# Kernel optimization log

Hardware: AMD Instinct MI355X
Metric: run time of the kernel (lower is better)

## Reference

```python
import jax, jax.numpy as jnp
import numpy as np

E = 1024
H = 16
F = 4096
EPS = 1e-5


def layer_norm(x, gamma, beta):
    mu = jnp.mean(x, axis=-1, keepdims=True)
    var = jnp.var(x, axis=-1, keepdims=True)
    return (x - mu) * jax.lax.rsqrt(var + EPS) * gamma + beta


def setup_inputs() -> dict:
    key = jax.random.key(0)
    ks = jax.random.split(key, 12)
    s = lambda d: 1.0 / np.sqrt(d)
    x = jax.random.normal(ks[0], (2, 2048, E), dtype=jnp.float32)
    Wq = jax.random.uniform(ks[1], (E, E), minval=-s(E), maxval=s(E))
    bq = jnp.zeros((E,), jnp.float32)
    Wk = jax.random.uniform(ks[2], (E, E), minval=-s(E), maxval=s(E))
    bk = jnp.zeros((E,), jnp.float32)
    Wv = jax.random.uniform(ks[3], (E, E), minval=-s(E), maxval=s(E))
    bv = jnp.zeros((E,), jnp.float32)
    Wo = jax.random.uniform(ks[4], (E, E), minval=-s(E), maxval=s(E))
    bo = jnp.zeros((E,), jnp.float32)
    g1 = jnp.ones((E,), jnp.float32)
    b1 = jnp.zeros((E,), jnp.float32)
    W1 = jax.random.uniform(ks[5], (E, F), minval=-s(E), maxval=s(E))
    bf1 = jnp.zeros((F,), jnp.float32)
    W2 = jax.random.uniform(ks[6], (F, E), minval=-s(F), maxval=s(F))
    bf2 = jnp.zeros((E,), jnp.float32)
    g2 = jnp.ones((E,), jnp.float32)
    b2 = jnp.zeros((E,), jnp.float32)
    return dict(x=x, Wq=Wq, bq=bq, Wk=Wk, bk=bk, Wv=Wv, bv=bv, Wo=Wo, bo=bo,
                g1=g1, b1=b1, W1=W1, bf1=bf1, W2=W2, bf2=bf2, g2=g2, b2=b2)


def reference(x, Wq, bq, Wk, bk, Wv, bv, Wo, bo, g1, b1, W1, bf1, W2, bf2, g2, b2):
    B, L, _ = x.shape
    Dh = E // H
    q = (x @ Wq + bq).reshape(B, L, H, Dh).transpose(0, 2, 1, 3)  # b h l d
    k = (x @ Wk + bk).reshape(B, L, H, Dh).transpose(0, 2, 1, 3)  # computed but unused (faithful to source)
    v = (x @ Wv + bv).reshape(B, L, H, Dh).transpose(0, 2, 1, 3)
    # NOTE: source computes scores as Q @ V^T (not K), scaled, then softmax
    scores = jnp.einsum('bhqd,bhkd->bhqk', q, v) / jnp.sqrt(jnp.float32(Dh))
    att = jax.nn.softmax(scores, axis=-1)
    ctx = jnp.einsum('bhqk,bhkd->bhqd', att, v)
    ctx = ctx.transpose(0, 2, 1, 3).reshape(B, L, E)
    att_out = ctx @ Wo + bo
    post_att = layer_norm(x + att_out, g1, b1)
    ff = jax.nn.relu(post_att @ W1 + bf1) @ W2 + bf2
    return layer_norm(post_att + ff, g2, b2)
```

## Files before the change

kernel.cpp:

```cpp
#include <hip/hip_runtime.h>
#include <stdint.h>

typedef unsigned short u16;
typedef __attribute__((ext_vector_type(8))) short short8;
typedef __attribute__((ext_vector_type(4))) float f32x4;
typedef __attribute__((ext_vector_type(4))) unsigned short u16x4;

#define TOKENS 4096
#define E_DIM 1024
#define F_DIM 4096
#define SEQ 2048
#define NH 16
#define DH 64

__device__ __forceinline__ u16 f2b(float f) {
  union { float f; unsigned u; } v; v.f = f;
  unsigned r = v.u + 0x7fffu + ((v.u >> 16) & 1u);
  return (u16)(r >> 16);
}

__device__ __forceinline__ void gl2lds16(const u16* g, u16* l) {
  __builtin_amdgcn_global_load_lds(
      (const __attribute__((address_space(1))) unsigned int*)(size_t)(g),
      (__attribute__((address_space(3))) unsigned int*)(unsigned int)(size_t)(l),
      16, 0, 0);
}


__global__ __launch_bounds__(256)
void transpose_w(const float* __restrict__ W, u16* __restrict__ Wt, int K, int N) {
  __shared__ float tile[32][33];
  const int kb = blockIdx.x * 32, nb = blockIdx.y * 32;
  const int tx = threadIdx.x & 31, ty = threadIdx.x >> 5;
#pragma unroll
  for (int i = 0; i < 32; i += 8)
    tile[ty + i][tx] = W[(size_t)(kb + ty + i) * N + nb + tx];
  __syncthreads();
#pragma unroll
  for (int i = 0; i < 32; i += 8)
    Wt[(size_t)(nb + ty + i) * K + kb + tx] = f2b(tile[tx][ty + i]);
}

__global__ __launch_bounds__(256)
void f32_to_bf16(const float* __restrict__ in, u16* __restrict__ out) {
  const int i = blockIdx.x * 256 + threadIdx.x;
  f32x4 f = ((const f32x4*)in)[i];
  u16x4 u;
#pragma unroll
  for (int j = 0; j < 4; j++) u[j] = f2b(f[j]);
  ((u16x4*)out)[i] = u;
}

__global__ __launch_bounds__(256)
void transpose_v(const u16* __restrict__ vsrc, u16* __restrict__ vt) {
  __shared__ u16 tile[64][66];
  const int kb = blockIdx.x * 64;
  const int bh = blockIdx.y;
  const int b = bh >> 4, h = bh & 15;
  {
    const int d = threadIdx.x & 63, r = threadIdx.x >> 6;
#pragma unroll
    for (int i = 0; i < 64; i += 4)
      tile[r + i][d] = vsrc[(size_t)(b * SEQ + kb + r + i) * E_DIM + h * DH + d];
  }
  __syncthreads();
  {
    const int pos = threadIdx.x & 63;
    const int srck = (pos & 3) * 16 + (pos >> 2);
#pragma unroll
    for (int j = 0; j < 64; j += 4) {
      const int d = (threadIdx.x >> 6) + j;
      vt[(size_t)(bh * DH + d) * SEQ + kb + pos] = tile[srck][d];
    }
  }
}

template <int RELU, int OUTBF>
__global__ __launch_bounds__(512)
void gemm256(const u16* __restrict__ A, const u16* __restrict__ Bt,
             const float* __restrict__ bias, void* __restrict__ Cout,
             int N, int K) {
  __shared__ __align__(16) u16 lds[3][2][8192];
  const int tid = threadIdx.x;
  const int lane = tid & 63, wave = tid >> 6;
  const int wm = wave >> 2, wn = wave & 3;
  const int l15 = lane & 15, g = lane >> 4;

  const int bid = blockIdx.x;
  const int xcd = bid & 7, idx = bid >> 3;
  const int mT = (xcd >> 2) * 8 + (idx >> 2);
  const int nT = (xcd & 3) * 4 + (idx & 3);
  const int mBlk = mT * 256, nBlk = nT * 256;

  const u16* Ab = A + (size_t)mBlk * K;
  const u16* Bb = Bt + (size_t)nBlk * K;

  const int srow = lane >> 2;
  const int scolx = ((lane & 3) ^ ((lane >> 3) & 3)) * 8;
  const u16* sa0 = Ab + (size_t)(wave * 16 + srow) * K + scolx;
  const u16* sa1 = Ab + (size_t)((8 + wave) * 16 + srow) * K + scolx;
  const u16* sb0 = Bb + (size_t)(wave * 16 + srow) * K + scolx;
  const u16* sb1 = Bb + (size_t)((8 + wave) * 16 + srow) * K + scolx;

  const int fo = l15 * 32 + ((g ^ ((l15 >> 1) & 3)) << 3);

  f32x4 acc[8][4] = {};

  const int NT = K >> 5;

#define STAGE_A(buf, t)                                             \
  {                                                                 \
    gl2lds16(sa0 + (size_t)(t) * 32, &lds[buf][0][wave * 512 + lane * 8]);       \
    gl2lds16(sa1 + (size_t)(t) * 32, &lds[buf][0][(8 + wave) * 512 + lane * 8]); \
  }
#define STAGE_B(buf, t)                                             \
  {                                                                 \
    gl2lds16(sb0 + (size_t)(t) * 32, &lds[buf][1][wave * 512 + lane * 8]);       \
    gl2lds16(sb1 + (size_t)(t) * 32, &lds[buf][1][(8 + wave) * 512 + lane * 8]); \
  }

  STAGE_A(0, 0) STAGE_B(0, 0)
  STAGE_A(1, 1) STAGE_B(1, 1)
  asm volatile("s_waitcnt vmcnt(4)" ::: "memory");
  asm volatile("s_barrier" ::: "memory");

  int buf = 0, sbuf = 2;
  for (int t = 0; t < NT; ++t) {
    const u16* As_ = &lds[buf][0][wm * (8 * 512)];
    const u16* Bs_ = &lds[buf][1][wn * (4 * 512)];

    short8 af[4], bfr[4];
#pragma unroll
    for (int i = 0; i < 4; i++)
      af[i] = *(const short8*)(As_ + i * 512 + fo);
#pragma unroll
    for (int i = 0; i < 4; i++)
      bfr[i] = *(const short8*)(Bs_ + i * 512 + fo);
    if (t + 2 < NT) STAGE_A(sbuf, t + 2)
    asm volatile("s_barrier" ::: "memory");
    asm volatile("s_waitcnt lgkmcnt(0)" ::: "memory");
    __builtin_amdgcn_sched_barrier(0);
    __builtin_amdgcn_s_setprio(1);
#pragma unroll
    for (int mg = 0; mg < 4; mg++)
#pragma unroll
      for (int ng = 0; ng < 4; ng++)
        acc[mg][ng] = __builtin_amdgcn_mfma_f32_16x16x32_bf16(af[mg], bfr[ng],
                                                              acc[mg][ng], 0, 0, 0);
    __builtin_amdgcn_s_setprio(0);
    asm volatile("s_barrier" ::: "memory");

#pragma unroll
    for (int i = 0; i < 4; i++)
      af[i] = *(const short8*)(As_ + (4 + i) * 512 + fo);
    if (t + 2 < NT) STAGE_B(sbuf, t + 2)
    asm volatile("s_barrier" ::: "memory");
    asm volatile("s_waitcnt lgkmcnt(0)" ::: "memory");
    __builtin_amdgcn_sched_barrier(0);
    __builtin_amdgcn_s_setprio(1);
#pragma unroll
    for (int mg = 0; mg < 4; mg++)
#pragma unroll
      for (int ng = 0; ng < 4; ng++)
        acc[4 + mg][ng] = __builtin_amdgcn_mfma_f32_16x16x32_bf16(af[mg], bfr[ng],
                                                                  acc[4 + mg][ng], 0, 0, 0);
    __builtin_amdgcn_s_setprio(0);
    if (t + 2 < NT) asm volatile("s_waitcnt vmcnt(4)" ::: "memory");
    else            asm volatile("s_waitcnt vmcnt(0)" ::: "memory");
    asm volatile("s_barrier" ::: "memory");

    buf = (buf == 2) ? 0 : buf + 1;
    sbuf = (sbuf == 2) ? 0 : sbuf + 1;
  }
#undef STAGE_A
#undef STAGE_B

  const int row0 = mBlk + wm * 128 + g * 4;
  const int col0 = nBlk + wn * 64 + l15;
#pragma unroll
  for (int ng = 0; ng < 4; ng++) {
    const int c = col0 + ng * 16;
    const float bv = bias[c];
#pragma unroll
    for (int mg = 0; mg < 8; mg++) {
#pragma unroll
      for (int r = 0; r < 4; r++) {
        float v = acc[mg][ng][r] + bv;
        if (RELU) v = fmaxf(v, 0.f);
        const size_t o = (size_t)(row0 + mg * 16 + r) * N + c;
        if (OUTBF) ((u16*)Cout)[o] = f2b(v);
        else       ((float*)Cout)[o] = v;
      }
    }
  }
}

__global__ __launch_bounds__(512)
void gemm_wide_sk(const u16* __restrict__ A, const u16* __restrict__ Bt,
                  const float* __restrict__ bias, float* __restrict__ Cout,
                  int N, int K) {
  __shared__ __align__(16) u16 lds[3][12288];
  const int tid = threadIdx.x;
  const int lane = tid & 63, wave = tid >> 6;
  const int wm = wave >> 1, wn = wave & 1;
  const int l15 = lane & 15, g = lane >> 4;

  const int bid = blockIdx.x;
  const int xcd = bid & 7, idx = bid >> 3;
  const int kz = xcd & 1;
  const int nT = ((xcd >> 1) & 1) * 4 + (idx & 3);
  const int mT = (xcd >> 2) * 8 + (idx >> 2);
  const int mBlk = mT * 256, nBlk = nT * 128;
  const int Kh = K >> 1;

  const u16* Ab = A + (size_t)mBlk * K + (size_t)kz * Kh;
  const u16* Bb = Bt + (size_t)nBlk * K + (size_t)kz * Kh;

  const int srow = lane >> 2;
  const int scolx = ((lane & 3) ^ ((lane >> 3) & 3)) * 8;
  const u16* sa0 = Ab + (size_t)(wave * 16 + srow) * K + scolx;
  const u16* sa1 = Ab + (size_t)((8 + wave) * 16 + srow) * K + scolx;
  const u16* sb0 = Bb + (size_t)(wave * 16 + srow) * K + scolx;

  const int fo = l15 * 32 + ((g ^ ((l15 >> 1) & 3)) << 3);

  f32x4 acc[4][4] = {};
  const int NT = Kh >> 5;

#define WSTAGE(buf, t)                                                         \
  {                                                                            \
    gl2lds16(sa0 + (size_t)(t) * 32, &lds[buf][wave * 512 + lane * 8]);        \
    gl2lds16(sa1 + (size_t)(t) * 32, &lds[buf][(8 + wave) * 512 + lane * 8]);  \
    gl2lds16(sb0 + (size_t)(t) * 32, &lds[buf][8192 + wave * 512 + lane * 8]); \
  }

  WSTAGE(0, 0)
  WSTAGE(1, 1)
  asm volatile("s_waitcnt vmcnt(3)" ::: "memory");
  asm volatile("s_barrier" ::: "memory");

  int buf = 0, sbuf = 2;
  for (int t = 0; t < NT; ++t) {
    const u16* As_ = &lds[buf][wm * (4 * 512)];
    const u16* Bs_ = &lds[buf][8192 + wn * (4 * 512)];
    short8 af[4], bfr[4];
#pragma unroll
    for (int i = 0; i < 4; i++)
      af[i] = *(const short8*)(As_ + i * 512 + fo);
#pragma unroll
    for (int i = 0; i < 4; i++)
      bfr[i] = *(const short8*)(Bs_ + i * 512 + fo);
    if (t + 2 < NT) WSTAGE(sbuf, t + 2)
    asm volatile("s_waitcnt lgkmcnt(0)" ::: "memory");
    __builtin_amdgcn_sched_barrier(0);
    __builtin_amdgcn_s_setprio(1);
#pragma unroll
    for (int mi = 0; mi < 4; mi++)
#pragma unroll
      for (int ni = 0; ni < 4; ni++)
        acc[mi][ni] = __builtin_amdgcn_mfma_f32_16x16x32_bf16(af[mi], bfr[ni],
                                                              acc[mi][ni], 0, 0, 0);
    __builtin_amdgcn_s_setprio(0);
    if (t + 2 < NT) asm volatile("s_waitcnt vmcnt(3)" ::: "memory");
    else            asm volatile("s_waitcnt vmcnt(0)" ::: "memory");
    asm volatile("s_barrier" ::: "memory");
    buf = (buf == 2) ? 0 : buf + 1;
    sbuf = (sbuf == 2) ? 0 : sbuf + 1;
  }
#undef WSTAGE

  float* out = Cout + (size_t)kz * TOKENS * N;
  const int row0 = mBlk + wm * 64 + g * 4;
  const int col0 = nBlk + wn * 64 + l15;
#pragma unroll
  for (int ni = 0; ni < 4; ni++) {
    const int c = col0 + ni * 16;
    const float bv = (kz == 0) ? bias[c] : 0.f;
#pragma unroll
    for (int mi = 0; mi < 4; mi++) {
#pragma unroll
      for (int r = 0; r < 4; r++)
        out[(size_t)(row0 + mi * 16 + r) * N + c] = acc[mi][ni][r] + bv;
    }
  }
}

__global__ __launch_bounds__(256)
void gemm_qv64(const u16* __restrict__ A, const u16* __restrict__ Bqv,
               const float* __restrict__ bq, const float* __restrict__ bv,
               u16* __restrict__ qout, u16* __restrict__ vout, int K) {
  __shared__ __align__(16) u16 lds[3][6144];
  const int tid = threadIdx.x;
  const int lane = tid & 63, wave = tid >> 6;
  const int mBlk = blockIdx.y * 128, nBlk = blockIdx.x * 64;
  const int isQ = nBlk < 1024;
  const int ncol = isQ ? nBlk : nBlk - 1024;
  const float* bias = isQ ? bq : bv;
  u16* out = isQ ? qout : vout;
  const float oscale = isQ ? 0.125f * 1.44269504088896f : 1.0f;
  const int wm = (wave >> 1) * 64, wn = (wave & 1) * 32;
  const int l15 = lane & 15, g = lane >> 4;

  f32x4 acc[4][2] = {};
  const int srow = lane >> 2;
  const int scolx = ((lane & 3) ^ ((lane >> 3) & 3)) * 8;
  const int fo = l15 * 32 + ((g ^ ((l15 >> 1) & 3)) << 3);

  const u16* Ab = A + (size_t)mBlk * K;
  const u16* Bb = Bqv + (size_t)nBlk * K;
  const u16* sa0 = Ab + (size_t)(wave * 16 + srow) * K + scolx;
  const u16* sa1 = Ab + (size_t)((4 + wave) * 16 + srow) * K + scolx;
  const u16* sb0 = Bb + (size_t)(wave * 16 + srow) * K + scolx;

  const int NT = K >> 5;

#define QSTAGE(buf, t)                                                         \
  {                                                                            \
    gl2lds16(sa0 + (size_t)(t) * 32, &lds[buf][wave * 512 + lane * 8]);        \
    gl2lds16(sa1 + (size_t)(t) * 32, &lds[buf][(4 + wave) * 512 + lane * 8]);  \
    gl2lds16(sb0 + (size_t)(t) * 32, &lds[buf][4096 + wave * 512 + lane * 8]); \
  }

  QSTAGE(0, 0)
  QSTAGE(1, 1)
  asm volatile("s_waitcnt vmcnt(3)" ::: "memory");
  asm volatile("s_barrier" ::: "memory");

  int buf = 0, sbuf = 2;
  for (int t = 0; t < NT; ++t) {
    const u16* As_ = &lds[buf][(wave >> 1) * (4 * 512)];
    const u16* Bs_ = &lds[buf][4096 + (wave & 1) * (2 * 512)];
    short8 af[4], bfr[2];
#pragma unroll
    for (int i = 0; i < 4; i++)
      af[i] = *(const short8*)(As_ + i * 512 + fo);
#pragma unroll
    for (int i = 0; i < 2; i++)
      bfr[i] = *(const short8*)(Bs_ + i * 512 + fo);
    if (t + 2 < NT) QSTAGE(sbuf, t + 2)
    asm volatile("s_waitcnt lgkmcnt(0)" ::: "memory");
    __builtin_amdgcn_sched_barrier(0);
    __builtin_amdgcn_s_setprio(1);
#pragma unroll
    for (int mi = 0; mi < 4; mi++)
#pragma unroll
      for (int ni = 0; ni < 2; ni++)
        acc[mi][ni] = __builtin_amdgcn_mfma_f32_16x16x32_bf16(af[mi], bfr[ni],
                                                              acc[mi][ni], 0, 0, 0);
    __builtin_amdgcn_s_setprio(0);
    if (t + 2 < NT) asm volatile("s_waitcnt vmcnt(3)" ::: "memory");
    else            asm volatile("s_waitcnt vmcnt(0)" ::: "memory");
    asm volatile("s_barrier" ::: "memory");
    buf = (buf == 2) ? 0 : buf + 1;
    sbuf = (sbuf == 2) ? 0 : sbuf + 1;
  }
#undef QSTAGE

  const int row0 = mBlk + wm + g * 4;
  const int col0 = ncol + wn + l15;
#pragma unroll
  for (int ni = 0; ni < 2; ni++) {
    const int c = col0 + ni * 16;
    const float bv_ = bias[c];
#pragma unroll
    for (int mi = 0; mi < 4; mi++) {
#pragma unroll
      for (int r = 0; r < 4; r++) {
        float v = (acc[mi][ni][r] + bv_) * oscale;
        out[(size_t)(row0 + mi * 16 + r) * E_DIM + c] = f2b(v);
      }
    }
  }
}

__global__ __launch_bounds__(256)
void attn_kernel(const u16* __restrict__ qb, const u16* __restrict__ vb,
                 const u16* __restrict__ vtb, u16* __restrict__ ctxb) {
  __shared__ __align__(16) u16 Vs[2][4096];
  __shared__ __align__(16) u16 Vts[2][4096];
  __shared__ __align__(16) u16 Pl[4][1024];
  const int tid = threadIdx.x;
  const int lane = tid & 63;
  const int wave = tid >> 6;
  const int l15 = lane & 15;
  const int g = lane >> 4;
  const int l7 = l15 & 7;
  const int qblk = blockIdx.x;
  const int bh = blockIdx.y;
  const int b = bh >> 4;
  const int h = bh & 15;
  const int qrow = qblk * 64 + wave * 16;

  short8 aq0, aq1;
  {
    const u16* qp = qb + ((size_t)(b * SEQ + qrow + l15)) * E_DIM + h * DH + g * 8;
    aq0 = *(const short8*)(qp);
    aq1 = *(const short8*)(qp + 32);
  }

  f32x4 o[4] = {};
  float lsum[4] = {};

  u16* myPl = Pl[wave];

  const u16* qk0b0 = Vs[0] + l15 * 64 + ((g ^ l7) * 8);
  const u16* qk1b0 = Vs[0] + l15 * 64 + (((4 + g) ^ l7) * 8);
  const u16* bv0b0 = Vts[0] + l15 * 64 + ((g ^ l7) * 8);
  const u16* bv1b0 = Vts[0] + l15 * 64 + (((4 + g) ^ l7) * 8);
  const u16* ap0 = myPl + l15 * 64 + ((g ^ l7) << 3);
  const u16* ap1 = myPl + l15 * 64 + (((4 + g) ^ l7) << 3);
  u16* wr0 = myPl + (g * 4 + 0) * 64 + (((l15 >> 1) ^ ((g * 4 + 0) & 7)) << 3) + ((l15 & 1) << 2);
  u16* wr1 = myPl + (g * 4 + 1) * 64 + (((l15 >> 1) ^ ((g * 4 + 1) & 7)) << 3) + ((l15 & 1) << 2);
  u16* wr2 = myPl + (g * 4 + 2) * 64 + (((l15 >> 1) ^ ((g * 4 + 2) & 7)) << 3) + ((l15 & 1) << 2);
  u16* wr3 = myPl + (g * 4 + 3) * 64 + (((l15 >> 1) ^ ((g * 4 + 3) & 7)) << 3) + ((l15 & 1) << 2);

  const int srow = tid >> 3;
  const int sch = tid & 7;
  const int r0 = srow, r1 = 32 + srow;
  const u16* pv0 = vb + ((size_t)(b * SEQ) + r0) * E_DIM + h * DH + ((sch ^ (r0 & 7)) * 8);
  const u16* pv1 = vb + ((size_t)(b * SEQ) + r1) * E_DIM + h * DH + ((sch ^ (r1 & 7)) * 8);
  const u16* pt0 = vtb + ((size_t)bh * DH + r0) * SEQ + ((sch ^ (r0 & 7)) * 8);
  const u16* pt1 = vtb + ((size_t)bh * DH + r1) * SEQ + ((sch ^ (r1 & 7)) * 8);

#define STAGE(buf)                                      \
  {                                                     \
    gl2lds16(pv0, Vs[buf] + tid * 8);                   \
    gl2lds16(pv1, Vs[buf] + 2048 + tid * 8);            \
    gl2lds16(pt0, Vts[buf] + tid * 8);                  \
    gl2lds16(pt1, Vts[buf] + 2048 + tid * 8);           \
    pv0 += 64 * E_DIM; pv1 += 64 * E_DIM;               \
    pt0 += 64; pt1 += 64;                               \
  }

#define SMROW(r, WR)                                                          \
  {                                                                           \
    union { float f; unsigned u; } p0, p1, p2, p3;                            \
    p0.f = __builtin_amdgcn_exp2f(s[0][r]);                                   \
    p1.f = __builtin_amdgcn_exp2f(s[1][r]);                                   \
    p2.f = __builtin_amdgcn_exp2f(s[2][r]);                                   \
    p3.f = __builtin_amdgcn_exp2f(s[3][r]);                                   \
    union { unsigned u; float f; } t0, t1, t2, t3;                            \
    t0.u = p0.u & 0xffff0000u; t1.u = p1.u & 0xffff0000u;                     \
    t2.u = p2.u & 0xffff0000u; t3.u = p3.u & 0xffff0000u;                     \
    lsum[r] += (t0.f + t1.f) + (t2.f + t3.f);                                 \
    uint2 pk;                                                                 \
    pk.x = __builtin_amdgcn_perm(p1.u, p0.u, 0x07060302u);                    \
    pk.y = __builtin_amdgcn_perm(p3.u, p2.u, 0x07060302u);                    \
    *(uint2*)(WR) = pk;                                                       \
  }

#define COMPUTE(QK0, QK1, BV0, BV1)                                           \
  {                                                                           \
    f32x4 s[4];                                                               \
    _Pragma("unroll") for (int nt = 0; nt < 4; nt++) {                        \
      short8 b0 = *(const short8*)((QK0) + nt * 1024);                        \
      short8 b1 = *(const short8*)((QK1) + nt * 1024);                        \
      f32x4 z = {};                                                           \
      z = __builtin_amdgcn_mfma_f32_16x16x32_bf16(aq0, b0, z, 0, 0, 0);       \
      z = __builtin_amdgcn_mfma_f32_16x16x32_bf16(aq1, b1, z, 0, 0, 0);       \
      s[nt] = z;                                                              \
    }                                                                         \
    SMROW(0, wr0) SMROW(1, wr1) SMROW(2, wr2) SMROW(3, wr3)                   \
    {                                                                         \
      short8 ap = *(const short8*)ap0;                                        \
      _Pragma("unroll") for (int dt = 0; dt < 4; dt++) {                      \
        short8 bvv = *(const short8*)((BV0) + dt * 1024);                     \
        o[dt] = __builtin_amdgcn_mfma_f32_16x16x32_bf16(ap, bvv, o[dt], 0, 0, 0); \
      }                                                                       \
      ap = *(const short8*)ap1;                                               \
      _Pragma("unroll") for (int dt = 0; dt < 4; dt++) {                      \
        short8 bvv = *(const short8*)((BV1) + dt * 1024);                     \
        o[dt] = __builtin_amdgcn_mfma_f32_16x16x32_bf16(ap, bvv, o[dt], 0, 0, 0); \
      }                                                                       \
    }                                                                         \
  }

#define HALF(CB, EN)                                                          \
  {                                                                           \
    asm volatile("s_barrier" ::: "memory");                                   \
    if (EN) {                                                                 \
      STAGE(CB ^ 1)                                                           \
      asm volatile("s_waitcnt vmcnt(4)" ::: "memory");                        \
    } else {                                                                  \
      asm volatile("s_waitcnt vmcnt(0)" ::: "memory");                        \
    }                                                                         \
    asm volatile("s_barrier" ::: "memory");                                   \
    if (CB == 0) { COMPUTE(qk0b0, qk1b0, bv0b0, bv1b0) }                      \
    else { COMPUTE(qk0b0 + 4096, qk1b0 + 4096, bv0b0 + 4096, bv1b0 + 4096) }  \
  }

  STAGE(0)
#pragma unroll 1
  for (int it = 0; it < 15; ++it) {
    HALF(0, 1)
    HALF(1, 1)
  }
  HALF(0, 1)
  HALF(1, 0)

#undef HALF
#undef COMPUTE
#undef SMROW
#undef STAGE

#pragma unroll
  for (int r = 0; r < 4; r++) {
    float l = lsum[r];
    l += __shfl_xor(l, 1);
    l += __shfl_xor(l, 2);
    l += __shfl_xor(l, 4);
    l += __shfl_xor(l, 8);
    const float inv = 1.0f / l;
    size_t base = ((size_t)(b * SEQ + qrow + g * 4 + r)) * E_DIM + h * DH;
#pragma unroll
    for (int dt = 0; dt < 4; dt++)
      ctxb[base + dt * 16 + l15] = f2b(o[dt][r] * inv);
  }
}

__global__ __launch_bounds__(256)
void add_ln3(const float* __restrict__ X, const float* __restrict__ Y0,
             const float* __restrict__ Y1,
             const float* __restrict__ gam, const float* __restrict__ bet,
             float* __restrict__ out32, u16* __restrict__ out16) {
  const int row = blockIdx.x;
  const int tid = threadIdx.x;
  const size_t base = (size_t)row * E_DIM;
  const int c4 = tid * 4;
  f32x4 x = *(const f32x4*)(X + base + c4);
  f32x4 y0 = *(const f32x4*)(Y0 + base + c4);
  f32x4 y1 = *(const f32x4*)(Y1 + base + c4);
  f32x4 v;
  float s = 0.f, sq = 0.f;
#pragma unroll
  for (int i = 0; i < 4; i++) {
    float t = x[i] + y0[i] + y1[i];
    v[i] = t; s += t; sq += t * t;
  }
#pragma unroll
  for (int off = 32; off; off >>= 1) {
    s += __shfl_xor(s, off);
    sq += __shfl_xor(sq, off);
  }
  __shared__ float sh[8];
  const int wave = tid >> 6, lane = tid & 63;
  if (lane == 0) { sh[wave] = s; sh[4 + wave] = sq; }
  __syncthreads();
  s = sh[0] + sh[1] + sh[2] + sh[3];
  sq = sh[4] + sh[5] + sh[6] + sh[7];
  const float mean = s * (1.f / 1024.f);
  const float var = sq * (1.f / 1024.f) - mean * mean;
  const float rstd = rsqrtf(var + 1e-5f);
  f32x4 gm = *(const f32x4*)(gam + c4);
  f32x4 bt = *(const f32x4*)(bet + c4);
  f32x4 y;
  u16x4 yb;
#pragma unroll
  for (int i = 0; i < 4; i++) {
    y[i] = (v[i] - mean) * rstd * gm[i] + bt[i];
    yb[i] = f2b(y[i]);
  }
  *(f32x4*)(out32 + base + c4) = y;
  if (out16) *(u16x4*)(out16 + base + c4) = yb;
}

extern "C" void kernel_launch(void* const* d_in, const int* in_sizes, int n_in,
                              void* d_out, int out_size, void* d_ws, size_t ws_size,
                              hipStream_t stream) {
  const float* x   = (const float*)d_in[0];
  const float* Wq  = (const float*)d_in[1];
  const float* bq  = (const float*)d_in[2];
  const float* Wv  = (const float*)d_in[5];
  const float* bv  = (const float*)d_in[6];
  const float* Wo  = (const float*)d_in[7];
  const float* bo  = (const float*)d_in[8];
  const float* g1  = (const float*)d_in[9];
  const float* b1  = (const float*)d_in[10];
  const float* W1  = (const float*)d_in[11];
  const float* bf1 = (const float*)d_in[12];
  const float* W2  = (const float*)d_in[13];
  const float* bf2 = (const float*)d_in[14];
  const float* g2  = (const float*)d_in[15];
  const float* b2  = (const float*)d_in[16];

  char* w = (char*)d_ws;
  const size_t MB = 1024ull * 1024ull;
  u16*   xb   = (u16*)(w + 0);
  u16*   h1   = (u16*)(w + 8 * MB);
  u16*   qb   = (u16*)(w + 8 * MB);
  u16*   vb   = (u16*)(w + 16 * MB);
  u16*   vtb  = (u16*)(w + 24 * MB);
  u16*   ctxb = (u16*)(w + 32 * MB);
  float* att0 = (float*)(w + 40 * MB);
  float* ff0  = (float*)(w + 40 * MB);
  float* pa   = (float*)(w + 72 * MB);
  u16*   pab  = (u16*)(w + 88 * MB);
  u16*   WqT  = (u16*)(w + 96 * MB);
  u16*   WvT  = (u16*)(w + 98 * MB);
  u16*   WoT  = (u16*)(w + 100 * MB);
  u16*   W1T  = (u16*)(w + 102 * MB);
  u16*   W2T  = (u16*)(w + 110 * MB);

  transpose_w<<<dim3(32, 32), 256, 0, stream>>>(Wq, WqT, 1024, 1024);
  transpose_w<<<dim3(32, 32), 256, 0, stream>>>(Wv, WvT, 1024, 1024);
  transpose_w<<<dim3(32, 32), 256, 0, stream>>>(Wo, WoT, 1024, 1024);
  transpose_w<<<dim3(32, 128), 256, 0, stream>>>(W1, W1T, 1024, 4096);
  transpose_w<<<dim3(128, 32), 256, 0, stream>>>(W2, W2T, 4096, 1024);
  f32_to_bf16<<<TOKENS * E_DIM / 4 / 256, 256, 0, stream>>>(x, xb);

  gemm_qv64<<<dim3(32, 32), 256, 0, stream>>>(xb, WqT, bq, bv, qb, vb, 1024);
  transpose_v<<<dim3(32, 32), 256, 0, stream>>>(vb, vtb);
  attn_kernel<<<dim3(32, 32), 256, 0, stream>>>(qb, vb, vtb, ctxb);
  gemm_wide_sk<<<dim3(256), 512, 0, stream>>>(ctxb, WoT, bo, att0, 1024, 1024);
  add_ln3<<<TOKENS, 256, 0, stream>>>(x, att0, att0 + (size_t)TOKENS * 1024, g1, b1, pa, pab);
  gemm256<1, 1><<<dim3(256), 512, 0, stream>>>(pab, W1T, bf1, h1, 4096, 1024);
  gemm_wide_sk<<<dim3(256), 512, 0, stream>>>(h1, W2T, bf2, ff0, 1024, 4096);
  add_ln3<<<TOKENS, 256, 0, stream>>>(pa, ff0, ff0 + (size_t)TOKENS * 1024, g2, b2, (float*)d_out, (u16*)nullptr);
}
```

Measured before the change: 359.2 us.

## Enlarge fused QV GEMM tiles to 256x128 with XCD-aware block mapping

The fused Q/V projection GEMM goes from 128x64 tiles with 256 threads (1024 blocks) to 256x128 tiles with 512 threads (256 blocks). Each wave now computes a 64x64 sub-tile, and the 1-D block index is remapped so blocks on the same XCD share A and B rows. The goal is more data reuse per LDS load and better L2 locality, at the cost of more registers, more LDS per block and only one wave of blocks across the CUs. The three 1024x1024 weight transposes are also merged into one launch with a z-dimension to cut launch overhead.

After: 343.2 us. 4.4% less time.

```diff
diff --git a/kernel.cpp b/kernel.cpp
--- a/kernel.cpp
+++ b/kernel.cpp
@@ -26,6 +26,24 @@
       16, 0, 0);
 }
 
+
+__global__ __launch_bounds__(256)
+void transpose_w3(const float* __restrict__ W0, const float* __restrict__ W1s,
+                  const float* __restrict__ W2s, u16* __restrict__ T0,
+                  u16* __restrict__ T1, u16* __restrict__ T2) {
+  __shared__ float tile[32][33];
+  const float* W = (blockIdx.z == 0) ? W0 : (blockIdx.z == 1) ? W1s : W2s;
+  u16* Wt = (blockIdx.z == 0) ? T0 : (blockIdx.z == 1) ? T1 : T2;
+  const int kb = blockIdx.x * 32, nb = blockIdx.y * 32;
+  const int tx = threadIdx.x & 31, ty = threadIdx.x >> 5;
+#pragma unroll
+  for (int i = 0; i < 32; i += 8)
+    tile[ty + i][tx] = W[(size_t)(kb + ty + i) * 1024 + nb + tx];
+  __syncthreads();
+#pragma unroll
+  for (int i = 0; i < 32; i += 8)
+    Wt[(size_t)(nb + ty + i) * 1024 + kb + tx] = f2b(tile[tx][ty + i]);
+}
 
 __global__ __launch_bounds__(256)
 void transpose_w(const float* __restrict__ W, u16* __restrict__ Wt, int K, int N) {
@@ -285,40 +303,47 @@
   }
 }
 
-__global__ __launch_bounds__(256)
-void gemm_qv64(const u16* __restrict__ A, const u16* __restrict__ Bqv,
-               const float* __restrict__ bq, const float* __restrict__ bv,
-               u16* __restrict__ qout, u16* __restrict__ vout, int K) {
-  __shared__ __align__(16) u16 lds[3][6144];
+__global__ __launch_bounds__(512)
+void gemm_qv(const u16* __restrict__ A, const u16* __restrict__ Bqv,
+             const float* __restrict__ bq, const float* __restrict__ bv,
+             u16* __restrict__ qout, u16* __restrict__ vout, int K) {
+  __shared__ __align__(16) u16 lds[3][12288];
   const int tid = threadIdx.x;
   const int lane = tid & 63, wave = tid >> 6;
-  const int mBlk = blockIdx.y * 128, nBlk = blockIdx.x * 64;
-  const int isQ = nBlk < 1024;
-  const int ncol = isQ ? nBlk : nBlk - 1024;
+  const int wm = wave >> 1, wn = wave & 1;
+  const int l15 = lane & 15, g = lane >> 4;
+
+  const int bid = blockIdx.x;
+  const int xcd = bid & 7, idx = bid >> 3;
+  const int mT = (xcd >> 1) * 4 + (idx >> 3);
+  const int nT = (xcd & 1) * 8 + (idx & 7);
+  const int mBlk = mT * 256, nBlkG = nT * 128;
+
+  const int isQ = nT < 8;
+  const int ncol = isQ ? nBlkG : nBlkG - 1024;
   const float* bias = isQ ? bq : bv;
   u16* out = isQ ? qout : vout;
   const float oscale = isQ ? 0.125f * 1.44269504088896f : 1.0f;
-  const int wm = (wave >> 1) * 64, wn = (wave & 1) * 32;
-  const int l15 = lane & 15, g = lane >> 4;
-
-  f32x4 acc[4][2] = {};
+
+  const u16* Ab = A + (size_t)mBlk * K;
+  const u16* Bb = Bqv + (size_t)nBlkG * K;
+
   const int srow = lane >> 2;
   const int scolx = ((lane & 3) ^ ((lane >> 3) & 3)) * 8;
+  const u16* sa0 = Ab + (size_t)(wave * 16 + srow) * K + scolx;
+  const u16* sa1 = Ab + (size_t)((8 + wave) * 16 + srow) * K + scolx;
+  const u16* sb0 = Bb + (size_t)(wave * 16 + srow) * K + scolx;
+
   const int fo = l15 * 32 + ((g ^ ((l15 >> 1) & 3)) << 3);
 
-  const u16* Ab = A + (size_t)mBlk * K;
-  const u16* Bb = Bqv + (size_t)nBlk * K;
-  const u16* sa0 = Ab + (size_t)(wave * 16 + srow) * K + scolx;
-  const u16* sa1 = Ab + (size_t)((4 + wave) * 16 + srow) * K + scolx;
-  const u16* sb0 = Bb + (size_t)(wave * 16 + srow) * K + scolx;
-
+  f32x4 acc[4][4] = {};
   const int NT = K >> 5;
 
 #define QSTAGE(buf, t)                                                         \
   {                                                                            \
     gl2lds16(sa0 + (size_t)(t) * 32, &lds[buf][wave * 512 + lane * 8]);        \
-    gl2lds16(sa1 + (size_t)(t) * 32, &lds[buf][(4 + wave) * 512 + lane * 8]);  \
-    gl2lds16(sb0 + (size_t)(t) * 32, &lds[buf][4096 + wave * 512 + lane * 8]); \
+    gl2lds16(sa1 + (size_t)(t) * 32, &lds[buf][(8 + wave) * 512 + lane * 8]);  \
+    gl2lds16(sb0 + (size_t)(t) * 32, &lds[buf][8192 + wave * 512 + lane * 8]); \
   }
 
   QSTAGE(0, 0)
@@ -328,14 +353,14 @@
 
   int buf = 0, sbuf = 2;
   for (int t = 0; t < NT; ++t) {
-    const u16* As_ = &lds[buf][(wave >> 1) * (4 * 512)];
-    const u16* Bs_ = &lds[buf][4096 + (wave & 1) * (2 * 512)];
-    short8 af[4], bfr[2];
+    const u16* As_ = &lds[buf][wm * (4 * 512)];
+    const u16* Bs_ = &lds[buf][8192 + wn * (4 * 512)];
+    short8 af[4], bfr[4];
 #pragma unroll
     for (int i = 0; i < 4; i++)
       af[i] = *(const short8*)(As_ + i * 512 + fo);
 #pragma unroll
-    for (int i = 0; i < 2; i++)
+    for (int i = 0; i < 4; i++)
       bfr[i] = *(const short8*)(Bs_ + i * 512 + fo);
     if (t + 2 < NT) QSTAGE(sbuf, t + 2)
     asm volatile("s_waitcnt lgkmcnt(0)" ::: "memory");
@@ -344,7 +369,7 @@
 #pragma unroll
     for (int mi = 0; mi < 4; mi++)
 #pragma unroll
-      for (int ni = 0; ni < 2; ni++)
+      for (int ni = 0; ni < 4; ni++)
         acc[mi][ni] = __builtin_amdgcn_mfma_f32_16x16x32_bf16(af[mi], bfr[ni],
                                                               acc[mi][ni], 0, 0, 0);
     __builtin_amdgcn_s_setprio(0);
@@ -356,10 +381,10 @@
   }
 #undef QSTAGE
 
-  const int row0 = mBlk + wm + g * 4;
-  const int col0 = ncol + wn + l15;
-#pragma unroll
-  for (int ni = 0; ni < 2; ni++) {
+  const int row0 = mBlk + wm * 64 + g * 4;
+  const int col0 = ncol + wn * 64 + l15;
+#pragma unroll
+  for (int ni = 0; ni < 4; ni++) {
     const int c = col0 + ni * 16;
     const float bv_ = bias[c];
 #pragma unroll
@@ -601,14 +626,12 @@
   u16*   W1T  = (u16*)(w + 102 * MB);
   u16*   W2T  = (u16*)(w + 110 * MB);
 
-  transpose_w<<<dim3(32, 32), 256, 0, stream>>>(Wq, WqT, 1024, 1024);
-  transpose_w<<<dim3(32, 32), 256, 0, stream>>>(Wv, WvT, 1024, 1024);
-  transpose_w<<<dim3(32, 32), 256, 0, stream>>>(Wo, WoT, 1024, 1024);
+  transpose_w3<<<dim3(32, 32, 3), 256, 0, stream>>>(Wq, Wv, Wo, WqT, WvT, WoT);
   transpose_w<<<dim3(32, 128), 256, 0, stream>>>(W1, W1T, 1024, 4096);
   transpose_w<<<dim3(128, 32), 256, 0, stream>>>(W2, W2T, 4096, 1024);
   f32_to_bf16<<<TOKENS * E_DIM / 4 / 256, 256, 0, stream>>>(x, xb);
 
-  gemm_qv64<<<dim3(32, 32), 256, 0, stream>>>(xb, WqT, bq, bv, qb, vb, 1024);
+  gemm_qv<<<dim3(256), 512, 0, stream>>>(xb, WqT, bq, bv, qb, vb, 1024);
   transpose_v<<<dim3(32, 32), 256, 0, stream>>>(vb, vtb);
   attn_kernel<<<dim3(32, 32), 256, 0, stream>>>(qb, vb, vtb, ctxb);
   gemm_wide_sk<<<dim3(256), 512, 0, stream>>>(ctxb, WoT, bo, att0, 1024, 1024);
```
